# Kernel optimization log

Hardware: AMD Instinct MI355X
Metric: run time of the kernel (lower is better)

The kernel has to match this reference:

```python
import jax, jax.numpy as jnp
import numpy as np

THR = 1.0      # spiking threshold for encoder and hidden LIF neurons
ALPHA = 0.9    # hidden membrane leak
BETA = 0.9     # output (leaky-integrator) membrane leak
SUR_K = 10.0   # surrogate-gradient sharpness (fwd unaffected)


def _spike(v):
    # Hard Heaviside in fwd, sigmoid surrogate in bwd (straight-through)
    sur = jax.nn.sigmoid(SUR_K * (v - THR))
    hard = (v >= THR).astype(v.dtype)
    return sur + jax.lax.stop_gradient(hard - sur)


def setup_inputs() -> dict:
    key = jax.random.key(0)
    k1, k2, k3 = jax.random.split(key, 3)
    B, T, ORDER, H, C = 512, 1024, 128, 1024, 10
    x = jax.random.normal(k1, (B, T, ORDER), dtype=jnp.float32)
    W_hdn = jax.random.normal(k2, (2 * ORDER, H), dtype=jnp.float32) * (1.0 / np.sqrt(2 * ORDER))
    W_otp = jax.random.normal(k3, (H, C), dtype=jnp.float32) * (1.0 / np.sqrt(H))
    return {"x": x, "W_hdn": W_hdn, "W_otp": W_otp}


def reference(x, W_hdn, W_otp):
    # x: (B, T, ORDER). States are reset (zeros) at the start of each forward,
    # mirroring reset_v()/reset_states() in the torch module.
    B, T, ORDER = x.shape
    H = W_hdn.shape[1]
    C = W_otp.shape[1]
    dt = x.dtype

    xt = jnp.transpose(x, (1, 0, 2))  # (T, B, ORDER) for scan

    def step(carry, x_t):
        v_e, v_h, v_o = carry
        # EncoderLayer: on/off rectified channels -> IF neuron with soft reset
        cur = jnp.concatenate([jax.nn.relu(x_t), jax.nn.relu(-x_t)], axis=-1)  # (B, 2*ORDER)
        v_e = v_e + cur
        s_e = _spike(v_e)
        v_e = v_e - s_e * THR
        # HiddenLayer: LIF with leak ALPHA, soft reset
        v_h = ALPHA * v_h + s_e @ W_hdn
        s_h = _spike(v_h)
        v_h = v_h - s_h * THR
        # OutputLayer: non-spiking leaky integrator; emit membrane potential
        v_o = BETA * v_o + s_h @ W_otp
        return (v_e, v_h, v_o), v_o

    init = (
        jnp.zeros((B, 2 * ORDER), dtype=dt),
        jnp.zeros((B, H), dtype=dt),
        jnp.zeros((B, C), dtype=dt),
    )
    _, m_pots = jax.lax.scan(step, init, xt)  # (T, B, C)
    return jnp.transpose(m_pots, (1, 0, 2))   # (B, T, C) == all_m_pots
```

## Files before the change

### kernel.cpp

```cpp
#include <hip/hip_runtime.h>
#include <hip/hip_bf16.h>


#define BB 512
#define TT 1024
#define OO 128
#define KK 256
#define HH 1024
#define CC 10
#define TC 64
#define NCHUNK (TT / TC)

typedef unsigned long long u64;
typedef __attribute__((ext_vector_type(8))) short short8;
typedef __attribute__((ext_vector_type(4))) float floatx4;
typedef __attribute__((ext_vector_type(4))) int intx4;

__device__ __forceinline__ unsigned short f2bf_rn(float f) {
    unsigned u = __float_as_uint(f);
    u += 0x7FFFu + ((u >> 16) & 1u);
    return (unsigned short)(u >> 16);
}
__device__ __forceinline__ float bf2f(unsigned short h) {
    return __uint_as_float(((unsigned)h) << 16);
}

__device__ __forceinline__ short8 bitsx8_bf16(unsigned e) {
    union { short8 s; unsigned u[4]; } r;
#pragma unroll
    for (int j = 0; j < 4; ++j) {
        unsigned t = (e >> (2 * j)) & 3u;
        r.u[j] = ((t | (t << 15)) & 0x10001u) * 0x3F80u;
    }
    return r.s;
}

__global__ __launch_bounds__(128) void k_enc(const float* __restrict__ x,
                                             u64* __restrict__ me) {
    const int b    = blockIdx.x;
    const int j    = threadIdx.x;
    const int wv   = j >> 6;
    const int lane = j & 63;
    const float* xb = x + (size_t)b * (TT * OO);
    float vp = 0.f, vn = 0.f;
    for (int t0 = 0; t0 < TT; t0 += 16) {
        float xs[16];
#pragma unroll
        for (int g = 0; g < 16; ++g) xs[g] = xb[(t0 + g) * OO + j];
#pragma unroll
        for (int g = 0; g < 16; ++g) {
            float xv = xs[g];
            float cp = fmaxf(xv, 0.f);
            float cn = fmaxf(-xv, 0.f);
            vp += cp;
            vn += cn;
            bool sp = (vp >= 1.0f);
            bool sn = (vn >= 1.0f);
            u64 mp = __ballot(sp);
            u64 mn = __ballot(sn);
            if (sp) vp -= 1.0f;
            if (sn) vn -= 1.0f;
            if (lane == 0) {
                size_t r = ((size_t)b * TT + (t0 + g)) * 4;
                me[r + wv]     = mp;
                me[r + 2 + wv] = mn;
            }
        }
    }
}

__global__ __launch_bounds__(256) void k_quant(const float* __restrict__ Wh,
                                               unsigned short* __restrict__ Wt) {
    int idx = blockIdx.x * 256 + threadIdx.x;
    int n = idx >> 9;
    int k = idx & 511;
    float w = Wh[(size_t)(k & 255) * HH + n];
    unsigned short hi = f2bf_rn(w);
    unsigned short out = (k < KK) ? hi : f2bf_rn(w - bf2f(hi));
    Wt[(size_t)n * 512 + k] = out;
}

__global__ __launch_bounds__(256) void k_quant_o(const float* __restrict__ Wo,
                                                 unsigned short* __restrict__ Wqo) {
    int idx = blockIdx.x * 256 + threadIdx.x;
    int n = idx >> 11;
    int k = idx & 2047;
    unsigned short out = 0;
    if (n < CC) {
        float w = Wo[(size_t)(k & 1023) * CC + n];
        unsigned short hi = f2bf_rn(w);
        out = (k < HH) ? hi : f2bf_rn(w - bf2f(hi));
    }
    Wqo[(size_t)n * 2048 + k] = out;
}

__global__ __launch_bounds__(256, 2) void k_gemm_scan(
    const u64* __restrict__ me, const unsigned short* __restrict__ Wt,
    u64* __restrict__ mh) {
    __shared__ __align__(16) char smem[66560];
    char* bufA = smem;
    char* bufB = smem + 16384;
    u64*  Mld  = (u64*)(smem + 32768);
    float* Scr = (float*)smem;

    const int tid  = threadIdx.x;
    const int wave = tid >> 6;
    const int lane = tid & 63;
    const int quad = lane >> 4;
    const int l15  = lane & 15;
    const int mtile = blockIdx.x;
    const int ny    = blockIdx.y;

    const int b = mtile * 4 + wave;
    float vh[2] = {0.f, 0.f};

    const int nl = tid >> 1, cpart = tid & 1;
    const unsigned short* wsrc = Wt + ((size_t)(ny * 128 + nl) * 512);
    char* wdstA = bufA + nl * 128;
    char* wdstB = bufB + nl * 128;

    for (int ct = 0; ct < NCHUNK; ++ct) {
        const int t0 = ct * TC;

        __syncthreads();
        {
            int m  = mtile * 256 + tid;
            int bb = m >> 6;
            int tl = m & 63;
            size_t base = ((size_t)bb * TT + (t0 + tl)) * 4;
#pragma unroll
            for (int w = 0; w < 4; ++w) Mld[w * 256 + tid] = me[base + w];
        }
        intx4 nxt[4];
#pragma unroll
        for (int p = 0; p < 4; ++p) nxt[p] = ((const intx4*)wsrc)[cpart * 4 + p];
#pragma unroll
        for (int p = 0; p < 4; ++p) {
            int jj = cpart * 4 + p;
            *((intx4*)(wdstA + ((jj ^ (nl & 7)) * 16))) = nxt[p];
        }
#pragma unroll
        for (int p = 0; p < 4; ++p) nxt[p] = ((const intx4*)(wsrc + 64))[cpart * 4 + p];
        __syncthreads();

        floatx4 acc[4][8];
#pragma unroll
        for (int i = 0; i < 4; ++i)
#pragma unroll
            for (int j2 = 0; j2 < 8; ++j2) acc[i][j2] = floatx4{0.f, 0.f, 0.f, 0.f};

#pragma unroll 2
        for (int kt = 0; kt < 8; ++kt) {
            char* rd  = (kt & 1) ? bufB : bufA;
            char* wrd = (kt & 1) ? wdstA : wdstB;
#pragma unroll
            for (int p = 0; p < 4; ++p) {
                int jj = cpart * 4 + p;
                *((intx4*)(wrd + ((jj ^ (nl & 7)) * 16))) = nxt[p];
            }
            int kn = (kt + 2 > 7) ? 7 : (kt + 2);
#pragma unroll
            for (int p = 0; p < 4; ++p)
                nxt[p] = ((const intx4*)(wsrc + kn * 64))[cpart * 4 + p];

            u64 aw[4];
#pragma unroll
            for (int mg = 0; mg < 4; ++mg)
                aw[mg] = Mld[(kt & 3) * 256 + wave * 64 + mg * 16 + l15];
#pragma unroll
            for (int kw = 0; kw < 2; ++kw) {
                int shift = kw * 32 + quad * 8;
                short8 afrag[4];
#pragma unroll
                for (int mg = 0; mg < 4; ++mg) {
                    unsigned byte = (unsigned)((aw[mg] >> shift) & 0xFFu);
                    afrag[mg] = bitsx8_bf16(byte);
                }
#pragma unroll
                for (int ng = 0; ng < 8; ++ng) {
                    int brow = ng * 16 + l15;
                    int jj = kw * 4 + quad;
                    short8 bfrag = *((const short8*)(rd + brow * 128 + ((jj ^ (brow & 7)) * 16)));
#pragma unroll
                    for (int mg = 0; mg < 4; ++mg)
                        acc[mg][ng] = __builtin_amdgcn_mfma_f32_16x16x32_bf16(
                            afrag[mg], bfrag, acc[mg][ng], 0, 0, 0);
                }
            }
            __syncthreads();
        }

        float* scr = Scr + wave * (64 * 65);
#pragma unroll
        for (int h = 0; h < 2; ++h) {
            __syncthreads();
#pragma unroll
            for (int mg = 0; mg < 4; ++mg)
#pragma unroll
                for (int ng2 = 0; ng2 < 4; ++ng2) {
                    int ng = h * 4 + ng2;
#pragma unroll
                    for (int r = 0; r < 4; ++r) {
                        int rowt = mg * 16 + quad * 4 + r;
                        int col  = ng2 * 16 + l15;
                        scr[rowt * 65 + col] = acc[mg][ng][r];
                    }
                }
            __syncthreads();
            float v = vh[h];
            for (int tl = 0; tl < TC; ++tl) {
                float c = scr[tl * 65 + lane];
                v = 0.9f * v + c;
                bool s = (v >= 1.0f);
                u64 wm = __ballot(s);
                if (s) v -= 1.0f;
                if (lane == 0) mh[((size_t)b * TT + (t0 + tl)) * 16 + ny * 2 + h] = wm;
            }
            vh[h] = v;
        }
    }
}

__global__ __launch_bounds__(256, 2) void k_outcur_mfma(
    const u64* __restrict__ mh, const unsigned short* __restrict__ Wqo,
    float* __restrict__ I) {
    __shared__ __align__(16) char smem[65536];
    char* Bo = smem;

    const int tid  = threadIdx.x;
    const int wave = tid >> 6;
    const int lane = tid & 63;
    const int quad = lane >> 4;
    const int l15  = lane & 15;

    {
#pragma unroll
        for (int i = 0; i < 16; ++i) {
            int pid = i * 256 + tid;
            int n = pid >> 8, p = pid & 255;
            intx4 v = ((const intx4*)Wqo)[pid];
            *((intx4*)(Bo + n * 4096 + ((p ^ (n & 7)) * 16))) = v;
        }
    }
    __syncthreads();

    const int tbase = blockIdx.x * 16 + wave * 4;
    floatx4 acc[4];
#pragma unroll
    for (int tt = 0; tt < 4; ++tt) acc[tt] = floatx4{0.f, 0.f, 0.f, 0.f};

    const u64* rowp[4];
#pragma unroll
    for (int tt = 0; tt < 4; ++tt)
        rowp[tt] = mh + ((size_t)(tbase + tt) * 16 + l15) * 16;

    for (int wi = 0; wi < 16; ++wi) {
        u64 w[4];
#pragma unroll
        for (int tt = 0; tt < 4; ++tt) w[tt] = rowp[tt][wi];
#pragma unroll
        for (int half = 0; half < 2; ++half) {
            int shift = half * 32 + quad * 8;
            int kt_hi = 2 * wi + half;
            int kt_lo = 32 + kt_hi;
            int j_hi = kt_hi * 4 + quad;
            int j_lo = kt_lo * 4 + quad;
            short8 bhi = *((const short8*)(Bo + l15 * 4096 + ((j_hi ^ (l15 & 7)) * 16)));
            short8 blo = *((const short8*)(Bo + l15 * 4096 + ((j_lo ^ (l15 & 7)) * 16)));
#pragma unroll
            for (int tt = 0; tt < 4; ++tt) {
                unsigned byte = (unsigned)((w[tt] >> shift) & 0xFFu);
                short8 af = bitsx8_bf16(byte);
                acc[tt] = __builtin_amdgcn_mfma_f32_16x16x32_bf16(af, bhi, acc[tt], 0, 0, 0);
                acc[tt] = __builtin_amdgcn_mfma_f32_16x16x32_bf16(af, blo, acc[tt], 0, 0, 0);
            }
        }
    }

#pragma unroll
    for (int tt = 0; tt < 4; ++tt)
#pragma unroll
        for (int r = 0; r < 4; ++r) {
            int m = (tbase + tt) * 16 + quad * 4 + r;
            if (l15 < CC) I[(size_t)m * CC + l15] = acc[tt][r];
        }
}

__global__ __launch_bounds__(192) void k_integ1(const float* __restrict__ I,
                                                float* __restrict__ out,
                                                float* __restrict__ vend) {
    int b = blockIdx.x;
    int tid = threadIdx.x;
    if (tid >= 160) return;
    int chunk = tid / 10, c = tid % 10;
    int t0 = chunk * 64;
    const float* Ib = I + ((size_t)b * TT + t0) * CC + c;
    float* ob = out + ((size_t)b * TT + t0) * CC + c;
    float v = 0.f;
    for (int g0 = 0; g0 < 64; g0 += 8) {
        float xs[8];
#pragma unroll
        for (int g = 0; g < 8; ++g) xs[g] = Ib[(g0 + g) * CC];
#pragma unroll
        for (int g = 0; g < 8; ++g) {
            v = 0.9f * v + xs[g];
            ob[(g0 + g) * CC] = v;
        }
    }
    vend[((size_t)b * 16 + chunk) * CC + c] = v;
}

__global__ __launch_bounds__(256) void k_integ2(const float* __restrict__ vend,
                                                float* __restrict__ carry) {
    int id = blockIdx.x * 256 + threadIdx.x;
    if (id >= BB * CC) return;
    int b = id / CC, c = id % CC;
    float d64 = 1.f;
#pragma unroll
    for (int i = 0; i < 64; ++i) d64 *= 0.9f;
    float cv = 0.f;
    for (int k = 0; k < 16; ++k) {
        carry[((size_t)b * 16 + k) * CC + c] = cv;
        cv = vend[((size_t)b * 16 + k) * CC + c] + d64 * cv;
    }
}

__global__ __launch_bounds__(256) void k_integ3(const float* __restrict__ carry,
                                                float* __restrict__ out) {
    __shared__ float dec[64];
    if (threadIdx.x == 0) {
        float d = 1.f;
        for (int i = 0; i < 64; ++i) { d *= 0.9f; dec[i] = d; }
    }
    __syncthreads();
    size_t id = (size_t)blockIdx.x * 256 + threadIdx.x;
    int c = (int)(id % CC);
    size_t bt = id / CC;
    int t = (int)(bt % TT);
    int b = (int)(bt / TT);
    int chunk = t >> 6, tl = t & 63;
    out[id] += dec[tl] * carry[((size_t)b * 16 + chunk) * CC + c];
}

extern "C" void kernel_launch(void* const* d_in, const int* in_sizes, int n_in,
                              void* d_out, int out_size, void* d_ws, size_t ws_size,
                              hipStream_t stream) {
    const float* x  = (const float*)d_in[0];
    const float* Wh = (const float*)d_in[1];
    const float* Wo = (const float*)d_in[2];

    char* p = (char*)d_ws;
    u64* me = (u64*)p;                        p += (size_t)BB * TT * 4 * 8;
    u64* mh = (u64*)p;                        p += (size_t)BB * TT * 16 * 8;
    unsigned short* Wt = (unsigned short*)p;  p += (size_t)HH * 512 * 2;
    float* I = (float*)p;                     p += (size_t)BB * TT * CC * 4;
    unsigned short* Wqo = (unsigned short*)p; p += (size_t)16 * 2048 * 2;
    float* vend  = (float*)Wt;
    float* carry = (float*)(Wt + 512 * 512);

    hipLaunchKernelGGL(k_enc, dim3(BB), dim3(128), 0, stream, x, me);
    hipLaunchKernelGGL(k_quant, dim3(2048), dim3(256), 0, stream, Wh, Wt);
    hipLaunchKernelGGL(k_quant_o, dim3(128), dim3(256), 0, stream, Wo, Wqo);
    hipLaunchKernelGGL(k_gemm_scan, dim3(128, 8), dim3(256), 0, stream, me, Wt, mh);
    hipLaunchKernelGGL(k_outcur_mfma, dim3(2048), dim3(256), 0, stream, mh, Wqo, I);
    hipLaunchKernelGGL(k_integ1, dim3(BB), dim3(192), 0, stream, I, (float*)d_out, vend);
    hipLaunchKernelGGL(k_integ2, dim3(20), dim3(256), 0, stream, vend, carry);
    hipLaunchKernelGGL(k_integ3, dim3(20480), dim3(256), 0, stream, carry, (float*)d_out);
}
```

Baseline: 1.160 ms.

## Stage weight tiles via global_load_lds and vectorize scan scratch with coalesced spike stores

Replaces the register-staged weight copies into LDS with direct global-to-LDS loads (global_load_lds) that prefetch the next k-tile, freeing registers and VALU work. The epilogue scratch is moved to a per-wave XOR-swizzled layout read back as float4 vectors, which removes the block-wide barriers around it. Spike masks are collected per lane and written once per chunk as a coalesced store instead of 64 serial lane-0 stores. LDS use grows to 72KB per block, which may limit occupancy to two blocks per CU.

Result: faster. 1.056 ms (-9.0%).

```diff
diff --git a/kernel.cpp b/kernel.cpp
--- a/kernel.cpp
+++ b/kernel.cpp
@@ -30,9 +30,22 @@
 #pragma unroll
     for (int j = 0; j < 4; ++j) {
         unsigned t = (e >> (2 * j)) & 3u;
-        r.u[j] = ((t | (t << 15)) & 0x10001u) * 0x3F80u;
+        r.u[j] = (((t << 15) | t) & 0x10001u) * 0x3F80u;
     }
     return r.s;
+}
+
+__device__ __forceinline__ void stage_kt(char* dstbuf ,
+                                         const unsigned short* gsrc ,
+                                         int kt) {
+#pragma unroll
+    for (int i = 0; i < 4; ++i) {
+        const unsigned short* g = gsrc + (size_t)i * 8 * 512 + kt * 64;
+        char* l = dstbuf + i * 1024;
+        __builtin_amdgcn_global_load_lds(
+            (const __attribute__((address_space(1))) unsigned int*)g,
+            (__attribute__((address_space(3))) unsigned int*)l, 16, 0, 0);
+    }
 }
 
 __global__ __launch_bounds__(128) void k_enc(const float* __restrict__ x,
@@ -97,11 +110,10 @@
 __global__ __launch_bounds__(256, 2) void k_gemm_scan(
     const u64* __restrict__ me, const unsigned short* __restrict__ Wt,
     u64* __restrict__ mh) {
-    __shared__ __align__(16) char smem[66560];
+    __shared__ __align__(16) char smem[73728];
     char* bufA = smem;
     char* bufB = smem + 16384;
-    u64*  Mld  = (u64*)(smem + 32768);
-    float* Scr = (float*)smem;
+    u64*  Mld  = (u64*)(smem + 65536);
 
     const int tid  = threadIdx.x;
     const int wave = tid >> 6;
@@ -114,15 +126,18 @@
     const int b = mtile * 4 + wave;
     float vh[2] = {0.f, 0.f};
 
-    const int nl = tid >> 1, cpart = tid & 1;
-    const unsigned short* wsrc = Wt + ((size_t)(ny * 128 + nl) * 512);
-    char* wdstA = bufA + nl * 128;
-    char* wdstB = bufB + nl * 128;
+    const unsigned short* gsrc =
+        Wt + (size_t)(ny * 128 + wave * 32 + (lane >> 3)) * 512 +
+        (((lane & 7) ^ (lane >> 3)) * 8);
+    char* dstA = bufA + wave * 4096;
+    char* dstB = bufB + wave * 4096;
+    float* scrw = (float*)(smem + wave * 16384);
 
     for (int ct = 0; ct < NCHUNK; ++ct) {
         const int t0 = ct * TC;
 
         __syncthreads();
+        stage_kt(dstA, gsrc, 0);
         {
             int m  = mtile * 256 + tid;
             int bb = m >> 6;
@@ -131,16 +146,6 @@
 #pragma unroll
             for (int w = 0; w < 4; ++w) Mld[w * 256 + tid] = me[base + w];
         }
-        intx4 nxt[4];
-#pragma unroll
-        for (int p = 0; p < 4; ++p) nxt[p] = ((const intx4*)wsrc)[cpart * 4 + p];
-#pragma unroll
-        for (int p = 0; p < 4; ++p) {
-            int jj = cpart * 4 + p;
-            *((intx4*)(wdstA + ((jj ^ (nl & 7)) * 16))) = nxt[p];
-        }
-#pragma unroll
-        for (int p = 0; p < 4; ++p) nxt[p] = ((const intx4*)(wsrc + 64))[cpart * 4 + p];
         __syncthreads();
 
         floatx4 acc[4][8];
@@ -151,17 +156,8 @@
 
 #pragma unroll 2
         for (int kt = 0; kt < 8; ++kt) {
-            char* rd  = (kt & 1) ? bufB : bufA;
-            char* wrd = (kt & 1) ? wdstA : wdstB;
-#pragma unroll
-            for (int p = 0; p < 4; ++p) {
-                int jj = cpart * 4 + p;
-                *((intx4*)(wrd + ((jj ^ (nl & 7)) * 16))) = nxt[p];
-            }
-            int kn = (kt + 2 > 7) ? 7 : (kt + 2);
-#pragma unroll
-            for (int p = 0; p < 4; ++p)
-                nxt[p] = ((const intx4*)(wsrc + kn * 64))[cpart * 4 + p];
+            char* rd = (kt & 1) ? bufB : bufA;
+            if (kt < 7) stage_kt((kt & 1) ? dstA : dstB, gsrc, kt + 1);
 
             u64 aw[4];
 #pragma unroll
@@ -190,32 +186,41 @@
             __syncthreads();
         }
 
-        float* scr = Scr + wave * (64 * 65);
 #pragma unroll
         for (int h = 0; h < 2; ++h) {
-            __syncthreads();
 #pragma unroll
             for (int mg = 0; mg < 4; ++mg)
 #pragma unroll
                 for (int ng2 = 0; ng2 < 4; ++ng2) {
-                    int ng = h * 4 + ng2;
+                    int nl = ng2 * 16 + l15;
+                    int p  = mg * 4 + quad;
+                    *((floatx4*)((char*)scrw + nl * 256 + ((p ^ l15) * 16))) =
+                        acc[mg][h * 4 + ng2];
+                }
+            float v = vh[h];
+            u64 mym = 0;
+#pragma unroll
+            for (int g = 0; g < 4; ++g) {
+                floatx4 cr[4];
+#pragma unroll
+                for (int q4 = 0; q4 < 4; ++q4) {
+                    int p = g * 4 + q4;
+                    cr[q4] = *((const floatx4*)((const char*)scrw + lane * 256 +
+                                                ((p ^ (lane & 15)) * 16)));
+                }
+#pragma unroll
+                for (int q4 = 0; q4 < 4; ++q4)
 #pragma unroll
                     for (int r = 0; r < 4; ++r) {
-                        int rowt = mg * 16 + quad * 4 + r;
-                        int col  = ng2 * 16 + l15;
-                        scr[rowt * 65 + col] = acc[mg][ng][r];
+                        int tl = g * 16 + q4 * 4 + r;
+                        v = 0.9f * v + cr[q4][r];
+                        bool s = (v >= 1.0f);
+                        u64 wm = __ballot(s);
+                        if (s) v -= 1.0f;
+                        if (lane == tl) mym = wm;
                     }
-                }
-            __syncthreads();
-            float v = vh[h];
-            for (int tl = 0; tl < TC; ++tl) {
-                float c = scr[tl * 65 + lane];
-                v = 0.9f * v + c;
-                bool s = (v >= 1.0f);
-                u64 wm = __ballot(s);
-                if (s) v -= 1.0f;
-                if (lane == 0) mh[((size_t)b * TT + (t0 + tl)) * 16 + ny * 2 + h] = wm;
             }
+            mh[((size_t)b * TT + (t0 + lane)) * 16 + ny * 2 + h] = mym;
             vh[h] = v;
         }
     }
```
